# Kernel optimization log

Hardware: AMD Instinct MI355X
Metric: run time of the kernel (lower is better)

## Reference

```python
import jax, jax.numpy as jnp
import numpy as np

S, D, H = 1024, 512, 4
DK = D // H  # 128
POOL = 16
EPS = 1e-5


def _pos_encoding(seq_len, dmodel):
    pos = jnp.arange(seq_len, dtype=jnp.float32)[:, None]
    div = jnp.exp(jnp.arange(0, dmodel, 2, dtype=jnp.float32) * (-jnp.log(10000.0) / dmodel))
    ang = pos * div  # [S, D/2]
    # interleave sin/cos -> pe[:,0::2]=sin, pe[:,1::2]=cos
    return jnp.stack([jnp.sin(ang), jnp.cos(ang)], axis=-1).reshape(seq_len, dmodel)


def _layernorm(x, g, b):
    mu = jnp.mean(x, axis=-1, keepdims=True)
    var = jnp.var(x, axis=-1, keepdims=True)
    return (x - mu) * jax.lax.rsqrt(var + EPS) * g + b


def setup_inputs() -> dict:
    key = jax.random.key(0)
    ks = jax.random.split(key, 16)
    u = lambda k, shape, r: jax.random.uniform(k, shape, jnp.float32, -r, r)
    nfeature = 512
    return {
        "x": jax.random.normal(ks[0], (16, S, nfeature), jnp.float32),
        "emb_w": u(ks[1], (nfeature, D), (1.0 / nfeature) ** 0.5),
        "emb_b": u(ks[2], (D,), (1.0 / nfeature) ** 0.5),
        "WQ": u(ks[3], (H, D, DK), 0.1),
        "WK": u(ks[4], (H, D, DK), 0.1),
        "WV": u(ks[5], (H, D, DK), 0.1),
        "WO": u(ks[6], (H * DK, D), 0.1),
        "g1": jnp.ones((D,), jnp.float32),
        "b1": jnp.zeros((D,), jnp.float32),
        "l1_w": u(ks[7], (D, 4 * D), (1.0 / D) ** 0.5),
        "l1_b": u(ks[8], (4 * D,), (1.0 / D) ** 0.5),
        "l2_w": u(ks[9], (4 * D, D), (1.0 / (4 * D)) ** 0.5),
        "l2_b": u(ks[10], (D,), (1.0 / (4 * D)) ** 0.5),
        "g2": jnp.ones((D,), jnp.float32),
        "b2": jnp.zeros((D,), jnp.float32),
        "fc_w": u(ks[11], (S * (D // POOL), 2), 0.1),
        "fc_b": jnp.zeros((2,), jnp.float32),
    }


def reference(x, emb_w, emb_b, WQ, WK, WV, WO, g1, b1, l1_w, l1_b, l2_w, l2_b, g2, b2, fc_w, fc_b):
    # dropout layers are identity (eval mode)
    h = x @ emb_w + emb_b                       # [B,S,D]
    h = h.reshape(-1, S, D) + _pos_encoding(S, D)
    inp = h
    # per-head projections (hand-rolled MHA)
    Qi = jnp.einsum('bsd,hde->bhse', h, WQ)     # [B,H,S,DK]
    Ki = jnp.einsum('bsd,hde->bhse', h, WK)
    Vi = jnp.einsum('bsd,hde->bhse', h, WV)
    scores = jnp.einsum('bhse,bhte->bhst', Qi, Ki) / jnp.sqrt(jnp.float32(DK))
    attn = jax.nn.softmax(scores, axis=-1)      # [B,H,S,S] -- full attention matrix, as in source
    head = jnp.einsum('bhst,bhte->bhse', attn, Vi)  # [B,H,S,DK]
    # NOTE: source does a raw reshape [B,H,S,DK] -> [B,S,H*DK] (no transpose); replicate exactly
    out = head.reshape(-1, S, H * DK) @ WO      # [B,S,D]
    h = _layernorm(out + inp, g1, b1)
    ffn = jax.nn.relu(h @ l1_w + l1_b) @ l2_w + l2_b
    h = _layernorm(ffn + h, g2, b2)
    # MaxPool1d(16,16) over the feature dim: [B,S,512] -> [B,S,32]
    pooled = h.reshape(-1, S, D // POOL, POOL).max(axis=-1)
    logits = pooled.reshape(-1, S * (D // POOL)) @ fc_w + fc_b  # [B,2]
    return jax.nn.log_softmax(logits, axis=-1)
```

## Files before the change

kernel.cpp:

```cpp
#include <hip/hip_runtime.h>

typedef unsigned short ushortb;
typedef __attribute__((ext_vector_type(8))) short short8;
typedef __attribute__((ext_vector_type(4))) float f32x4;

__device__ __forceinline__ ushortb f2bb(float f) {
    union { float f; unsigned u; } x; x.f = f;
    unsigned r = x.u + 0x7fffu + ((x.u >> 16) & 1u);
    return (ushortb)(r >> 16);
}
__device__ __forceinline__ float bb2f(ushortb u) {
    union { unsigned u; float f; } x; x.u = ((unsigned)u) << 16; return x.f;
}

__device__ __forceinline__ void async_ld16(void* lds, const void* g) {
    __builtin_amdgcn_global_load_lds(
        (const __attribute__((address_space(1))) void*)g,
        (__attribute__((address_space(3))) void*)lds, 16, 0, 0);
}

#define EP_EMB       0
#define EP_RES       2
#define EP_BIAS_RELU 3
#define EP_BIAS_RES  4
#define EP_QKV       7

template <int EP>
__global__ __launch_bounds__(256) void gemm_mfma(
    const ushortb* __restrict__ A, const ushortb* __restrict__ Bt,
    const float* __restrict__ bias, const ushortb* __restrict__ res,
    const float* __restrict__ pe, ushortb* __restrict__ C,
    int M, int N, int K)
{
    __shared__ ushortb sA[128][64];
    __shared__ ushortb sB[128][64];

    const int tid = threadIdx.x;
    const int wave = tid >> 6, lane = tid & 63;
    const int quad = lane >> 4, l15 = lane & 15;
    const int row0 = blockIdx.x * 128;
    const int col0 = blockIdx.y * 128;
    const int wm = (wave >> 1) * 64, wn = (wave & 1) * 64;
    const int srl = lane >> 3, slot = lane & 7;

    f32x4 acc[4][4];
    #pragma unroll
    for (int i = 0; i < 4; ++i)
        #pragma unroll
        for (int j = 0; j < 4; ++j) acc[i][j] = (f32x4){0.f, 0.f, 0.f, 0.f};

    for (int k0 = 0; k0 < K; k0 += 64) {
        __syncthreads();
        #pragma unroll
        for (int c = 0; c < 4; ++c) {
            int rbase = wave * 32 + c * 8;
            int r = rbase + srl;
            int ka = (slot ^ ((r ^ (r >> 3)) & 7)) * 8;
            async_ld16(&sA[rbase][0], A  + (size_t)(row0 + r) * K + k0 + ka);
            async_ld16(&sB[rbase][0], Bt + (size_t)(col0 + r) * K + k0 + ka);
        }
        __syncthreads();

        #pragma unroll
        for (int kc = 0; kc < 2; ++kc) {
            short8 af[4], bf[4];
            #pragma unroll
            for (int i = 0; i < 4; ++i) {
                int m = wm + i * 16 + l15;
                af[i] = *(const short8*)&sA[m][(((kc * 4 + quad) ^ ((m ^ (m >> 3)) & 7))) * 8];
            }
            #pragma unroll
            for (int j = 0; j < 4; ++j) {
                int n = wn + j * 16 + l15;
                bf[j] = *(const short8*)&sB[n][(((kc * 4 + quad) ^ ((n ^ (n >> 3)) & 7))) * 8];
            }
            #pragma unroll
            for (int i = 0; i < 4; ++i)
                #pragma unroll
                for (int j = 0; j < 4; ++j)
                    acc[i][j] = __builtin_amdgcn_mfma_f32_16x16x32_bf16(af[i], bf[j], acc[i][j], 0, 0, 0);
        }
    }

    if constexpr (EP == EP_QKV) {
        if (col0 < 1024) {
            ushortb* dst = C + ((size_t)(col0 >> 9)) * ((size_t)M * 512);
            #pragma unroll
            for (int i = 0; i < 4; ++i) {
                #pragma unroll
                for (int r = 0; r < 4; ++r) {
                    int row = row0 + wm + i * 16 + quad * 4 + r;
                    #pragma unroll
                    for (int j = 0; j < 4; ++j) {
                        int col = (col0 + wn + j * 16 + l15) & 511;
                        dst[(size_t)row * 512 + col] = f2bb(acc[i][j][r]);
                    }
                }
            }
        } else {
            ushortb* Vt = C + (size_t)2 * M * 512;
            int bb = row0 >> 10;
            #pragma unroll
            for (int i = 0; i < 4; ++i) {
                int s = (row0 & 1023) + wm + i * 16 + quad * 4;
                #pragma unroll
                for (int j = 0; j < 4; ++j) {
                    int vcol = col0 + wn + j * 16 + l15 - 1024;
                    int h = vcol >> 7, e = vcol & 127;
                    ushort4 v;
                    v.x = f2bb(acc[i][j][0]); v.y = f2bb(acc[i][j][1]);
                    v.z = f2bb(acc[i][j][2]); v.w = f2bb(acc[i][j][3]);
                    *(ushort4*)&Vt[((size_t)((bb * 4 + h) * 128 + e) << 10) + s] = v;
                }
            }
        }
        return;
    }

    #pragma unroll
    for (int i = 0; i < 4; ++i) {
        #pragma unroll
        for (int r = 0; r < 4; ++r) {
            int row = row0 + wm + i * 16 + quad * 4 + r;
            #pragma unroll
            for (int j = 0; j < 4; ++j) {
                int col = col0 + wn + j * 16 + l15;
                float v = acc[i][j][r];
                if constexpr (EP == EP_EMB) {
                    v += bias[col] + pe[((row & 1023) << 9) + col];
                } else if constexpr (EP == EP_RES) {
                    v += bb2f(res[(size_t)row * N + col]);
                } else if constexpr (EP == EP_BIAS_RELU) {
                    v = fmaxf(v + bias[col], 0.0f);
                } else if constexpr (EP == EP_BIAS_RES) {
                    v += bias[col] + bb2f(res[(size_t)row * N + col]);
                }
                C[(size_t)row * N + col] = f2bb(v);
            }
        }
    }
}

__global__ __launch_bounds__(256) void conv_x(const float* __restrict__ in,
                                              ushortb* __restrict__ out)
{
    size_t i4 = (size_t)blockIdx.x * 256 + threadIdx.x;
    float4 v = *(const float4*)(in + i4 * 4);
    ushort4 o;
    o.x = f2bb(v.x); o.y = f2bb(v.y); o.z = f2bb(v.z); o.w = f2bb(v.w);
    *(ushort4*)(out + i4 * 4) = o;
}

__global__ __launch_bounds__(256) void tileT(const float* __restrict__ in,
                                             ushortb* __restrict__ out,
                                             int R, int C, float scale)
{
    __shared__ float t[64][65];
    const int tx = threadIdx.x & 63, ty = threadIdx.x >> 6;
    const int c0 = blockIdx.x * 64, r0 = blockIdx.y * 64;
    const size_t zoff = (size_t)blockIdx.z * R * C;
    #pragma unroll
    for (int i = 0; i < 16; ++i) {
        int r = ty + i * 4;
        t[r][tx] = in[zoff + (size_t)(r0 + r) * C + c0 + tx] * scale;
    }
    __syncthreads();
    #pragma unroll
    for (int i = 0; i < 16; ++i) {
        int r = ty + i * 4;
        out[zoff + (size_t)(c0 + r) * R + r0 + tx] = f2bb(t[tx][r]);
    }
}

__global__ __launch_bounds__(256) void pe_kernel(float* __restrict__ pe)
{
    int idx = blockIdx.x * 256 + threadIdx.x;
    int s = idx >> 9, c = idx & 511;
    float div = expf((float)(c & ~1) * (-9.210340371976184f / 512.0f));
    float ang = (float)s * div;
    pe[idx] = (c & 1) ? cosf(ang) : sinf(ang);
}

__global__ __launch_bounds__(256) void attn_mfma(
    const ushortb* __restrict__ Qb, const ushortb* __restrict__ Kb,
    const ushortb* __restrict__ Vt, ushortb* __restrict__ O)
{
    __shared__ ushortb sK[32][136];
    __shared__ ushortb sVt[128][40];
    __shared__ ushortb sP[4][32][40];

    const int tid = threadIdx.x;
    const int wave = tid >> 6, lane = tid & 63;
    const int quad = lane >> 4, l15 = lane & 15;
    const int b = blockIdx.z, h = blockIdx.y;
    const int q0 = blockIdx.x * 128 + wave * 32;
    const size_t qk_off = ((size_t)b << 10) * 512 + h * 128;
    const ushortb* Qp = Qb + qk_off;
    const ushortb* Kp = Kb + qk_off;
    const ushortb* Vp = Vt + (((size_t)(b * 4 + h)) << 17);

    short8 qfA[4], qfB[4];
    {
        const ushortb* qa = Qp + (size_t)(q0 + l15) * 512;
        const ushortb* qb = Qp + (size_t)(q0 + 16 + l15) * 512;
        #pragma unroll
        for (int kc = 0; kc < 4; ++kc) {
            qfA[kc] = *(const short8*)(qa + kc * 32 + quad * 8);
            qfB[kc] = *(const short8*)(qb + kc * 32 + quad * 8);
        }
    }

    f32x4 oA[8], oB[8];
    #pragma unroll
    for (int dt = 0; dt < 8; ++dt) {
        oA[dt] = (f32x4){0.f, 0.f, 0.f, 0.f};
        oB[dt] = (f32x4){0.f, 0.f, 0.f, 0.f};
    }
    float lA = 0.f, lB = 0.f;

    for (int t0 = 0; t0 < 1024; t0 += 32) {
        __syncthreads();
        #pragma unroll
        for (int c = 0; c < 2; ++c) {
            int idx = c * 2048 + tid * 8;
            int t = idx >> 7, d0 = idx & 127;
            *(short8*)&sK[t][d0] = *(const short8*)(Kp + (size_t)(t0 + t) * 512 + d0);
        }
        #pragma unroll
        for (int c = 0; c < 2; ++c) {
            int idx = c * 256 + tid;
            int d = idx >> 2, toff = (idx & 3) * 8;
            *(short8*)&sVt[d][toff] = *(const short8*)(Vp + ((size_t)d << 10) + t0 + toff);
        }
        __syncthreads();

        f32x4 sA0 = {0,0,0,0}, sA1 = {0,0,0,0}, sB0 = {0,0,0,0}, sB1 = {0,0,0,0};
        #pragma unroll
        for (int kc = 0; kc < 4; ++kc) {
            short8 k0f = *(const short8*)&sK[l15][kc * 32 + quad * 8];
            short8 k1f = *(const short8*)&sK[16 + l15][kc * 32 + quad * 8];
            sA0 = __builtin_amdgcn_mfma_f32_16x16x32_bf16(k0f, qfA[kc], sA0, 0, 0, 0);
            sA1 = __builtin_amdgcn_mfma_f32_16x16x32_bf16(k1f, qfA[kc], sA1, 0, 0, 0);
            sB0 = __builtin_amdgcn_mfma_f32_16x16x32_bf16(k0f, qfB[kc], sB0, 0, 0, 0);
            sB1 = __builtin_amdgcn_mfma_f32_16x16x32_bf16(k1f, qfB[kc], sB1, 0, 0, 0);
        }

        float pA0[4], pA1[4], pB0[4], pB1[4];
        float sumA = 0.f, sumB = 0.f;
        #pragma unroll
        for (int r = 0; r < 4; ++r) {
            pA0[r] = exp2f(sA0[r]); pA1[r] = exp2f(sA1[r]);
            pB0[r] = exp2f(sB0[r]); pB1[r] = exp2f(sB1[r]);
            sumA += pA0[r] + pA1[r];
            sumB += pB0[r] + pB1[r];
        }
        lA += sumA; lB += sumB;

        ushort4 w;
        w.x = f2bb(pA0[0]); w.y = f2bb(pA0[1]); w.z = f2bb(pA0[2]); w.w = f2bb(pA0[3]);
        *(ushort4*)&sP[wave][l15][quad * 4] = w;
        w.x = f2bb(pA1[0]); w.y = f2bb(pA1[1]); w.z = f2bb(pA1[2]); w.w = f2bb(pA1[3]);
        *(ushort4*)&sP[wave][l15][16 + quad * 4] = w;
        w.x = f2bb(pB0[0]); w.y = f2bb(pB0[1]); w.z = f2bb(pB0[2]); w.w = f2bb(pB0[3]);
        *(ushort4*)&sP[wave][16 + l15][quad * 4] = w;
        w.x = f2bb(pB1[0]); w.y = f2bb(pB1[1]); w.z = f2bb(pB1[2]); w.w = f2bb(pB1[3]);
        *(ushort4*)&sP[wave][16 + l15][16 + quad * 4] = w;

        short8 pfA = *(const short8*)&sP[wave][l15][quad * 8];
        short8 pfB = *(const short8*)&sP[wave][16 + l15][quad * 8];

        #pragma unroll
        for (int dt = 0; dt < 8; ++dt) {
            short8 vfrag = *(const short8*)&sVt[dt * 16 + l15][quad * 8];
            oA[dt] = __builtin_amdgcn_mfma_f32_16x16x32_bf16(pfA, vfrag, oA[dt], 0, 0, 0);
            oB[dt] = __builtin_amdgcn_mfma_f32_16x16x32_bf16(pfB, vfrag, oB[dt], 0, 0, 0);
        }
    }

    lA += __shfl_xor(lA, 16); lA += __shfl_xor(lA, 32);
    lB += __shfl_xor(lB, 16); lB += __shfl_xor(lB, 32);

    const size_t obase = (((size_t)(b * 4 + h) << 10) + q0) << 7;
    #pragma unroll
    for (int r = 0; r < 4; ++r) {
        float invA = 1.0f / __shfl(lA, quad * 4 + r);
        float invB = 1.0f / __shfl(lB, quad * 4 + r);
        int qa = quad * 4 + r, qb = 16 + quad * 4 + r;
        #pragma unroll
        for (int dt = 0; dt < 8; ++dt) {
            O[obase + ((size_t)qa << 7) + dt * 16 + l15] = f2bb(oA[dt][r] * invA);
            O[obase + ((size_t)qb << 7) + dt * 16 + l15] = f2bb(oB[dt][r] * invB);
        }
    }
}

__global__ __launch_bounds__(256) void ln_kernel(const ushortb* __restrict__ in,
                                                 const float* __restrict__ g,
                                                 const float* __restrict__ bta,
                                                 ushortb* __restrict__ out)
{
    const int lane = threadIdx.x & 63, w = threadIdx.x >> 6;
    const size_t row = (size_t)blockIdx.x * 4 + w;
    const int e0 = lane * 8;
    short8 v8 = *(const short8*)(in + row * 512 + e0);
    float v[8];
    #pragma unroll
    for (int k = 0; k < 8; ++k) v[k] = bb2f((ushortb)((short*)&v8)[k]);
    float s = 0.f, sq = 0.f;
    #pragma unroll
    for (int k = 0; k < 8; ++k) { s += v[k]; sq += v[k] * v[k]; }
    #pragma unroll
    for (int o = 1; o < 64; o <<= 1) { s += __shfl_xor(s, o); sq += __shfl_xor(sq, o); }
    float mu = s * (1.0f / 512.0f);
    float var = sq * (1.0f / 512.0f) - mu * mu;
    float rstd = rsqrtf(var + 1e-5f);
    float4 g0 = *(const float4*)(g + e0),  g1 = *(const float4*)(g + e0 + 4);
    float4 b0 = *(const float4*)(bta + e0), b1 = *(const float4*)(bta + e0 + 4);
    float gg[8] = {g0.x, g0.y, g0.z, g0.w, g1.x, g1.y, g1.z, g1.w};
    float bb[8] = {b0.x, b0.y, b0.z, b0.w, b1.x, b1.y, b1.z, b1.w};
    short8 o8;
    #pragma unroll
    for (int k = 0; k < 8; ++k)
        ((short*)&o8)[k] = (short)f2bb((v[k] - mu) * rstd * gg[k] + bb[k]);
    *(short8*)(out + row * 512 + e0) = o8;
}

__global__ __launch_bounds__(256) void final_partial(const ushortb* __restrict__ ln2,
                                                     const float* __restrict__ fcw,
                                                     float* __restrict__ zbuf)
{
    const int b = blockIdx.x, chunk = blockIdx.y;
    const int tid = threadIdx.x;
    float a0 = 0.0f, a1 = 0.0f;
    #pragma unroll
    for (int t = 0; t < 8; ++t) {
        int m = chunk * 2048 + t * 256 + tid;
        int s = m >> 5, j = m & 31;
        const ushortb* p = ln2 + (((size_t)(b * 1024 + s)) << 9) + j * 16;
        float mx = -1e30f;
        #pragma unroll
        for (int e = 0; e < 16; ++e) mx = fmaxf(mx, bb2f(p[e]));
        a0 += mx * fcw[2 * m];
        a1 += mx * fcw[2 * m + 1];
    }
    __shared__ float r0[256], r1[256];
    r0[tid] = a0; r1[tid] = a1;
    __syncthreads();
    for (int o = 128; o > 0; o >>= 1) {
        if (tid < o) { r0[tid] += r0[tid + o]; r1[tid] += r1[tid + o]; }
        __syncthreads();
    }
    if (tid == 0) {
        atomicAdd(&zbuf[2 * b],     r0[0]);
        atomicAdd(&zbuf[2 * b + 1], r1[0]);
    }
}

__global__ __launch_bounds__(64) void final_logits(const float* __restrict__ zbuf,
                                                   const float* __restrict__ fcb,
                                                   float* __restrict__ out)
{
    int b = threadIdx.x;
    if (b < 16) {
        float z0 = zbuf[2 * b]     + fcb[0];
        float z1 = zbuf[2 * b + 1] + fcb[1];
        float mx = fmaxf(z0, z1);
        float lse = mx + logf(expf(z0 - mx) + expf(z1 - mx));
        out[2 * b]     = z0 - lse;
        out[2 * b + 1] = z1 - lse;
    }
}

extern "C" void kernel_launch(void* const* d_in, const int* in_sizes, int n_in,
                              void* d_out, int out_size, void* d_ws, size_t ws_size,
                              hipStream_t stream)
{
    const float* x     = (const float*)d_in[0];
    const float* emb_w = (const float*)d_in[1];
    const float* emb_b = (const float*)d_in[2];
    const float* WQ    = (const float*)d_in[3];
    const float* WK    = (const float*)d_in[4];
    const float* WV    = (const float*)d_in[5];
    const float* WO    = (const float*)d_in[6];
    const float* g1    = (const float*)d_in[7];
    const float* b1    = (const float*)d_in[8];
    const float* l1w   = (const float*)d_in[9];
    const float* l1b   = (const float*)d_in[10];
    const float* l2w   = (const float*)d_in[11];
    const float* l2b   = (const float*)d_in[12];
    const float* g2    = (const float*)d_in[13];
    const float* b2    = (const float*)d_in[14];
    const float* fcw   = (const float*)d_in[15];
    const float* fcb   = (const float*)d_in[16];
    float* out = (float*)d_out;

    char* ws = (char*)d_ws;
    const size_t Ub = (size_t)16384 * 512 * 2;
    ushortb* xb    = (ushortb*)(ws + 0 * Ub);
    ushortb* h0b   = (ushortb*)(ws + 1 * Ub);
    ushortb* Qb    = (ushortb*)(ws + 2 * Ub);
    ushortb* Kb    = (ushortb*)(ws + 3 * Ub);
    ushortb* Vt    = (ushortb*)(ws + 4 * Ub);
    ushortb* headR = (ushortb*)(ws + 5 * Ub);
    ushortb* mid   = (ushortb*)(ws + 3 * Ub);
    ushortb* r1    = xb;
    ushortb* ln1   = Qb;
    ushortb* r2    = xb;
    ushortb* ln2   = h0b;
    char* wb = ws + 7 * Ub;
    ushortb* embwt = (ushortb*)(wb);
    ushortb* wqkvt = (ushortb*)(wb + 524288);
    ushortb* wot   = (ushortb*)(wb + 2097152);
    ushortb* l1wt  = (ushortb*)(wb + 2621440);
    ushortb* l2wt  = (ushortb*)(wb + 4718592);
    float*   pe    = (float*)  (wb + 6815744);
    float*   zbuf  = (float*)  (wb + 8912896);

    const int M = 16384;
    const float qscale = 0.12753139626997592f;

    conv_x<<<8192, 256, 0, stream>>>(x, xb);
    pe_kernel<<<2048, 256, 0, stream>>>(pe);
    tileT<<<dim3(8, 8, 1),  256, 0, stream>>>(emb_w, embwt, 512, 512, 1.0f);
    tileT<<<dim3(2, 8, 4),  256, 0, stream>>>(WQ, wqkvt,               512, 128, qscale);
    tileT<<<dim3(2, 8, 4),  256, 0, stream>>>(WK, wqkvt + 262144,      512, 128, 1.0f);
    tileT<<<dim3(2, 8, 4),  256, 0, stream>>>(WV, wqkvt + 524288,      512, 128, 1.0f);
    tileT<<<dim3(8, 8, 1),  256, 0, stream>>>(WO, wot, 512, 512, 1.0f);
    tileT<<<dim3(32, 8, 1), 256, 0, stream>>>(l1w, l1wt, 512, 2048, 1.0f);
    tileT<<<dim3(8, 32, 1), 256, 0, stream>>>(l2w, l2wt, 2048, 512, 1.0f);
    hipMemsetAsync(zbuf, 0, 16 * 2 * sizeof(float), stream);

    gemm_mfma<EP_EMB><<<dim3(M / 128, 4), 256, 0, stream>>>(
        xb, embwt, emb_b, nullptr, pe, h0b, M, 512, 512);

    gemm_mfma<EP_QKV><<<dim3(M / 128, 12), 256, 0, stream>>>(
        h0b, wqkvt, nullptr, nullptr, nullptr, Qb, M, 1536, 512);

    attn_mfma<<<dim3(8, 4, 16), 256, 0, stream>>>(Qb, Kb, Vt, headR);

    gemm_mfma<EP_RES><<<dim3(M / 128, 4), 256, 0, stream>>>(
        headR, wot, nullptr, h0b, nullptr, r1, M, 512, 512);
    ln_kernel<<<M / 4, 256, 0, stream>>>(r1, g1, b1, ln1);

    gemm_mfma<EP_BIAS_RELU><<<dim3(M / 128, 16), 256, 0, stream>>>(
        ln1, l1wt, l1b, nullptr, nullptr, mid, M, 2048, 512);
    gemm_mfma<EP_BIAS_RES><<<dim3(M / 128, 4), 256, 0, stream>>>(
        mid, l2wt, l2b, ln1, nullptr, r2, M, 512, 2048);
    ln_kernel<<<M / 4, 256, 0, stream>>>(r2, g2, b2, ln2);

    final_partial<<<dim3(16, 16), 256, 0, stream>>>(ln2, fcw, zbuf);
    final_logits<<<1, 64, 0, stream>>>(zbuf, fcb, out);
}
```

Before: 390.4 us.

## Fold embedding into QKV weights and fuse embedding with QKV GEMM

Precomputes the product of the QKV projection weights and the embedding weights, plus a positional-encoding/bias table projected through QKV. A single GEMM over x then produces h0 and Q/K/V directly, removing the dependent embedding-to-QKV GEMM chain and one full activation round trip. The attention kernel now loads K/V tiles with async global-to-LDS copies into XOR-swizzled unpadded shared arrays, and uses a flat block index that puts heads of the same batch in adjacent blocks. The precomposed weights and tables are rounded to bf16, which changes numerics slightly.

Measured after the change: 408.6 us. 4.7% more time.

```diff
diff --git a/kernel.cpp b/kernel.cpp
--- a/kernel.cpp
+++ b/kernel.cpp
@@ -19,18 +19,18 @@
         (__attribute__((address_space(3))) void*)lds, 16, 0, 0);
 }
 
-#define EP_EMB       0
+#define EP_ST        1
 #define EP_RES       2
 #define EP_BIAS_RELU 3
 #define EP_BIAS_RES  4
-#define EP_QKV       7
+#define EP_MEGA      8
 
 template <int EP>
 __global__ __launch_bounds__(256) void gemm_mfma(
     const ushortb* __restrict__ A, const ushortb* __restrict__ Bt,
     const float* __restrict__ bias, const ushortb* __restrict__ res,
-    const float* __restrict__ pe, ushortb* __restrict__ C,
-    int M, int N, int K)
+    const ushortb* __restrict__ tab1, const ushortb* __restrict__ tab2,
+    ushortb* __restrict__ C, int M, int N, int K)
 {
     __shared__ ushortb sA[128][64];
     __shared__ ushortb sB[128][64];
@@ -82,35 +82,53 @@
         }
     }
 
-    if constexpr (EP == EP_QKV) {
-        if (col0 < 1024) {
-            ushortb* dst = C + ((size_t)(col0 >> 9)) * ((size_t)M * 512);
-            #pragma unroll
-            for (int i = 0; i < 4; ++i) {
+    if constexpr (EP == EP_MEGA) {
+        if (col0 < 512) {
+            #pragma unroll
+            for (int i = 0; i < 4; ++i)
                 #pragma unroll
                 for (int r = 0; r < 4; ++r) {
                     int row = row0 + wm + i * 16 + quad * 4 + r;
+                    int s = row & 1023;
                     #pragma unroll
                     for (int j = 0; j < 4; ++j) {
-                        int col = (col0 + wn + j * 16 + l15) & 511;
-                        dst[(size_t)row * 512 + col] = f2bb(acc[i][j][r]);
+                        int col = col0 + wn + j * 16 + l15;
+                        C[(size_t)row * 512 + col] =
+                            f2bb(acc[i][j][r] + bb2f(tab1[(s << 9) + col]));
                     }
                 }
-            }
+        } else if (col0 < 1536) {
+            int sec = (col0 - 512) >> 9;
+            ushortb* dst = C + (size_t)(1 + sec) * M * 512;
+            #pragma unroll
+            for (int i = 0; i < 4; ++i)
+                #pragma unroll
+                for (int r = 0; r < 4; ++r) {
+                    int row = row0 + wm + i * 16 + quad * 4 + r;
+                    int s = row & 1023;
+                    #pragma unroll
+                    for (int j = 0; j < 4; ++j) {
+                        int cn = col0 + wn + j * 16 + l15 - 512;
+                        dst[(size_t)row * 512 + (cn & 511)] =
+                            f2bb(acc[i][j][r] + bb2f(tab2[(size_t)s * 1536 + cn]));
+                    }
+                }
         } else {
-            ushortb* Vt = C + (size_t)2 * M * 512;
-            int bb = row0 >> 10;
+            ushortb* Vt = C + (size_t)3 * M * 512;
+            int bb_ = row0 >> 10;
             #pragma unroll
             for (int i = 0; i < 4; ++i) {
-                int s = (row0 & 1023) + wm + i * 16 + quad * 4;
+                int sb = (row0 & 1023) + wm + i * 16 + quad * 4;
                 #pragma unroll
                 for (int j = 0; j < 4; ++j) {
-                    int vcol = col0 + wn + j * 16 + l15 - 1024;
-                    int h = vcol >> 7, e = vcol & 127;
+                    int cn = col0 + wn + j * 16 + l15 - 512;
+                    int e = cn & 127, hh = (cn - 1024) >> 7;
                     ushort4 v;
-                    v.x = f2bb(acc[i][j][0]); v.y = f2bb(acc[i][j][1]);
-                    v.z = f2bb(acc[i][j][2]); v.w = f2bb(acc[i][j][3]);
-                    *(ushort4*)&Vt[((size_t)((bb * 4 + h) * 128 + e) << 10) + s] = v;
+                    v.x = f2bb(acc[i][j][0] + bb2f(tab2[(size_t)(sb + 0) * 1536 + cn]));
+                    v.y = f2bb(acc[i][j][1] + bb2f(tab2[(size_t)(sb + 1) * 1536 + cn]));
+                    v.z = f2bb(acc[i][j][2] + bb2f(tab2[(size_t)(sb + 2) * 1536 + cn]));
+                    v.w = f2bb(acc[i][j][3] + bb2f(tab2[(size_t)(sb + 3) * 1536 + cn]));
+                    *(ushort4*)&Vt[((size_t)((bb_ * 4 + hh) * 128 + e) << 10) + sb] = v;
                 }
             }
         }
@@ -126,9 +144,7 @@
             for (int j = 0; j < 4; ++j) {
                 int col = col0 + wn + j * 16 + l15;
                 float v = acc[i][j][r];
-                if constexpr (EP == EP_EMB) {
-                    v += bias[col] + pe[((row & 1023) << 9) + col];
-                } else if constexpr (EP == EP_RES) {
+                if constexpr (EP == EP_RES) {
                     v += bb2f(res[(size_t)row * N + col]);
                 } else if constexpr (EP == EP_BIAS_RELU) {
                     v = fmaxf(v + bias[col], 0.0f);
@@ -141,7 +157,7 @@
     }
 }
 
-__global__ __launch_bounds__(256) void conv_x(const float* __restrict__ in,
+__global__ __launch_bounds__(256) void conv_b(const float* __restrict__ in,
                                               ushortb* __restrict__ out)
 {
     size_t i4 = (size_t)blockIdx.x * 256 + threadIdx.x;
@@ -172,28 +188,32 @@
     }
 }
 
-__global__ __launch_bounds__(256) void pe_kernel(float* __restrict__ pe)
+__global__ __launch_bounds__(256) void peb_kernel(const float* __restrict__ emb_b,
+                                                  ushortb* __restrict__ peb)
 {
     int idx = blockIdx.x * 256 + threadIdx.x;
     int s = idx >> 9, c = idx & 511;
     float div = expf((float)(c & ~1) * (-9.210340371976184f / 512.0f));
     float ang = (float)s * div;
-    pe[idx] = (c & 1) ? cosf(ang) : sinf(ang);
+    float v = ((c & 1) ? cosf(ang) : sinf(ang)) + emb_b[c];
+    peb[idx] = f2bb(v);
 }
 
 __global__ __launch_bounds__(256) void attn_mfma(
     const ushortb* __restrict__ Qb, const ushortb* __restrict__ Kb,
     const ushortb* __restrict__ Vt, ushortb* __restrict__ O)
 {
-    __shared__ ushortb sK[32][136];
-    __shared__ ushortb sVt[128][40];
+    __shared__ ushortb sK[32][128];
+    __shared__ ushortb sVt[128][32];
     __shared__ ushortb sP[4][32][40];
 
     const int tid = threadIdx.x;
     const int wave = tid >> 6, lane = tid & 63;
     const int quad = lane >> 4, l15 = lane & 15;
-    const int b = blockIdx.z, h = blockIdx.y;
-    const int q0 = blockIdx.x * 128 + wave * 32;
+    const int bid = blockIdx.x;
+    const int bh = bid & 63, qc = bid >> 6;
+    const int b = bh >> 2, h = bh & 3;
+    const int q0 = qc * 128 + wave * 32;
     const size_t qk_off = ((size_t)b << 10) * 512 + h * 128;
     const ushortb* Qp = Qb + qk_off;
     const ushortb* Kp = Kb + qk_off;
@@ -222,23 +242,21 @@
         __syncthreads();
         #pragma unroll
         for (int c = 0; c < 2; ++c) {
-            int idx = c * 2048 + tid * 8;
-            int t = idx >> 7, d0 = idx & 127;
-            *(short8*)&sK[t][d0] = *(const short8*)(Kp + (size_t)(t0 + t) * 512 + d0);
-        }
-        #pragma unroll
-        for (int c = 0; c < 2; ++c) {
-            int idx = c * 256 + tid;
-            int d = idx >> 2, toff = (idx & 3) * 8;
-            *(short8*)&sVt[d][toff] = *(const short8*)(Vp + ((size_t)d << 10) + t0 + toff);
+            int seg = wave * 2 + c;
+            int rk = seg * 4 + (lane >> 4);
+            int ck = (lane & 15) ^ (rk & 15);
+            async_ld16(&sK[seg * 4][0], Kp + (size_t)(t0 + rk) * 512 + ck * 8);
+            int dv = seg * 16 + (lane >> 2);
+            int cv = (lane & 3) ^ (dv & 3);
+            async_ld16(&sVt[seg * 16][0], Vp + ((size_t)dv << 10) + t0 + cv * 8);
         }
         __syncthreads();
 
         f32x4 sA0 = {0,0,0,0}, sA1 = {0,0,0,0}, sB0 = {0,0,0,0}, sB1 = {0,0,0,0};
         #pragma unroll
         for (int kc = 0; kc < 4; ++kc) {
-            short8 k0f = *(const short8*)&sK[l15][kc * 32 + quad * 8];
-            short8 k1f = *(const short8*)&sK[16 + l15][kc * 32 + quad * 8];
+            short8 k0f = *(const short8*)&sK[l15][((kc * 4 + quad) ^ l15) * 8];
+            short8 k1f = *(const short8*)&sK[16 + l15][((kc * 4 + quad) ^ l15) * 8];
             sA0 = __builtin_amdgcn_mfma_f32_16x16x32_bf16(k0f, qfA[kc], sA0, 0, 0, 0);
             sA1 = __builtin_amdgcn_mfma_f32_16x16x32_bf16(k1f, qfA[kc], sA1, 0, 0, 0);
             sB0 = __builtin_amdgcn_mfma_f32_16x16x32_bf16(k0f, qfB[kc], sB0, 0, 0, 0);
@@ -271,7 +289,8 @@
 
         #pragma unroll
         for (int dt = 0; dt < 8; ++dt) {
-            short8 vfrag = *(const short8*)&sVt[dt * 16 + l15][quad * 8];
+            int d = dt * 16 + l15;
+            short8 vfrag = *(const short8*)&sVt[d][(quad ^ (d & 3)) * 8];
             oA[dt] = __builtin_amdgcn_mfma_f32_16x16x32_bf16(pfA, vfrag, oA[dt], 0, 0, 0);
             oB[dt] = __builtin_amdgcn_mfma_f32_16x16x32_bf16(pfB, vfrag, oB[dt], 0, 0, 0);
         }
@@ -408,44 +427,50 @@
     ushortb* r2    = xb;
     ushortb* ln2   = h0b;
     char* wb = ws + 7 * Ub;
-    ushortb* embwt = (ushortb*)(wb);
-    ushortb* wqkvt = (ushortb*)(wb + 524288);
-    ushortb* wot   = (ushortb*)(wb + 2097152);
-    ushortb* l1wt  = (ushortb*)(wb + 2621440);
-    ushortb* l2wt  = (ushortb*)(wb + 4718592);
-    float*   pe    = (float*)  (wb + 6815744);
-    float*   zbuf  = (float*)  (wb + 8912896);
+    ushortb* WB    = (ushortb*)(wb);
+    ushortb* W2t   = WB + (size_t)512 * 512;
+    ushortb* wqkvt = (ushortb*)(wb + 2097152);
+    ushortb* embc  = (ushortb*)(wb + 3670016);
+    ushortb* wot   = (ushortb*)(wb + 4194304);
+    ushortb* l1wt  = (ushortb*)(wb + 4718592);
+    ushortb* l2wt  = (ushortb*)(wb + 6815744);
+    ushortb* peb   = (ushortb*)(wb + 8912896);
+    ushortb* peqkv = (ushortb*)(wb + 9961472);
+    float*   zbuf  = (float*)  (wb + 13107200);
 
     const int M = 16384;
     const float qscale = 0.12753139626997592f;
 
-    conv_x<<<8192, 256, 0, stream>>>(x, xb);
-    pe_kernel<<<2048, 256, 0, stream>>>(pe);
-    tileT<<<dim3(8, 8, 1),  256, 0, stream>>>(emb_w, embwt, 512, 512, 1.0f);
-    tileT<<<dim3(2, 8, 4),  256, 0, stream>>>(WQ, wqkvt,               512, 128, qscale);
-    tileT<<<dim3(2, 8, 4),  256, 0, stream>>>(WK, wqkvt + 262144,      512, 128, 1.0f);
-    tileT<<<dim3(2, 8, 4),  256, 0, stream>>>(WV, wqkvt + 524288,      512, 128, 1.0f);
+    conv_b<<<8192, 256, 0, stream>>>(x, xb);
+    conv_b<<<256, 256, 0, stream>>>(emb_w, embc);
+    peb_kernel<<<2048, 256, 0, stream>>>(emb_b, peb);
+    tileT<<<dim3(8, 8, 1),  256, 0, stream>>>(emb_w, WB, 512, 512, 1.0f);
+    tileT<<<dim3(2, 8, 4),  256, 0, stream>>>(WQ, wqkvt,          512, 128, qscale);
+    tileT<<<dim3(2, 8, 4),  256, 0, stream>>>(WK, wqkvt + 262144, 512, 128, 1.0f);
+    tileT<<<dim3(2, 8, 4),  256, 0, stream>>>(WV, wqkvt + 524288, 512, 128, 1.0f);
     tileT<<<dim3(8, 8, 1),  256, 0, stream>>>(WO, wot, 512, 512, 1.0f);
     tileT<<<dim3(32, 8, 1), 256, 0, stream>>>(l1w, l1wt, 512, 2048, 1.0f);
     tileT<<<dim3(8, 32, 1), 256, 0, stream>>>(l2w, l2wt, 2048, 512, 1.0f);
     hipMemsetAsync(zbuf, 0, 16 * 2 * sizeof(float), stream);
 
-    gemm_mfma<EP_EMB><<<dim3(M / 128, 4), 256, 0, stream>>>(
-        xb, embwt, emb_b, nullptr, pe, h0b, M, 512, 512);
-
-    gemm_mfma<EP_QKV><<<dim3(M / 128, 12), 256, 0, stream>>>(
-        h0b, wqkvt, nullptr, nullptr, nullptr, Qb, M, 1536, 512);
-
-    attn_mfma<<<dim3(8, 4, 16), 256, 0, stream>>>(Qb, Kb, Vt, headR);
+    gemm_mfma<EP_ST><<<dim3(12, 4), 256, 0, stream>>>(
+        wqkvt, embc, nullptr, nullptr, nullptr, nullptr, W2t, 1536, 512, 512);
+    gemm_mfma<EP_ST><<<dim3(8, 12), 256, 0, stream>>>(
+        peb, wqkvt, nullptr, nullptr, nullptr, nullptr, peqkv, 1024, 1536, 512);
+
+    gemm_mfma<EP_MEGA><<<dim3(M / 128, 16), 256, 0, stream>>>(
+        xb, WB, nullptr, nullptr, peb, peqkv, h0b, M, 2048, 512);
+
+    attn_mfma<<<512, 256, 0, stream>>>(Qb, Kb, Vt, headR);
 
     gemm_mfma<EP_RES><<<dim3(M / 128, 4), 256, 0, stream>>>(
-        headR, wot, nullptr, h0b, nullptr, r1, M, 512, 512);
+        headR, wot, nullptr, h0b, nullptr, nullptr, r1, M, 512, 512);
     ln_kernel<<<M / 4, 256, 0, stream>>>(r1, g1, b1, ln1);
 
     gemm_mfma<EP_BIAS_RELU><<<dim3(M / 128, 16), 256, 0, stream>>>(
-        ln1, l1wt, l1b, nullptr, nullptr, mid, M, 2048, 512);
+        ln1, l1wt, l1b, nullptr, nullptr, nullptr, mid, M, 2048, 512);
     gemm_mfma<EP_BIAS_RES><<<dim3(M / 128, 4), 256, 0, stream>>>(
-        mid, l2wt, l2b, ln1, nullptr, r2, M, 512, 2048);
+        mid, l2wt, l2b, ln1, nullptr, nullptr, r2, M, 512, 2048);
     ln_kernel<<<M / 4, 256, 0, stream>>>(r2, g2, b2, ln2);
 
     final_partial<<<dim3(16, 16), 256, 0, stream>>>(ln2, fcw, zbuf);
```

## Double-buffer LDS tiles in GEMM and attention to overlap loads with MFMA

Applied to the files above, without the earlier changes.

The GEMM main loop now uses two LDS buffers. The next K-tile is prefetched with global_load_lds while MFMAs run on the current one, which leaves one barrier per iteration instead of two. The attention kernel gets the same treatment: K and V^T tiles move to double-buffered async LDS loads, and an XOR swizzle replaces the row padding to avoid bank conflicts. The attention grid is also flattened to 1D so that blocks sharing a batch and head are spread differently across CUs. In exchange, GEMM LDS use doubles to 64KB per block, which can lower occupancy.

New measurement: 367.3 us. 5.9% less time.

```diff
diff --git a/kernel.cpp b/kernel.cpp
--- a/kernel.cpp
+++ b/kernel.cpp
@@ -32,8 +32,8 @@
     const float* __restrict__ pe, ushortb* __restrict__ C,
     int M, int N, int K)
 {
-    __shared__ ushortb sA[128][64];
-    __shared__ ushortb sB[128][64];
+    __shared__ ushortb sA[2][128][64];
+    __shared__ ushortb sB[2][128][64];
 
     const int tid = threadIdx.x;
     const int wave = tid >> 6, lane = tid & 63;
@@ -49,30 +49,41 @@
         #pragma unroll
         for (int j = 0; j < 4; ++j) acc[i][j] = (f32x4){0.f, 0.f, 0.f, 0.f};
 
+    #pragma unroll
+    for (int c = 0; c < 4; ++c) {
+        int rbase = wave * 32 + c * 8;
+        int r = rbase + srl;
+        int ka = (slot ^ ((r ^ (r >> 3)) & 7)) * 8;
+        async_ld16(&sA[0][rbase][0], A  + (size_t)(row0 + r) * K + ka);
+        async_ld16(&sB[0][rbase][0], Bt + (size_t)(col0 + r) * K + ka);
+    }
+
+    int buf = 0;
     for (int k0 = 0; k0 < K; k0 += 64) {
         __syncthreads();
-        #pragma unroll
-        for (int c = 0; c < 4; ++c) {
-            int rbase = wave * 32 + c * 8;
-            int r = rbase + srl;
-            int ka = (slot ^ ((r ^ (r >> 3)) & 7)) * 8;
-            async_ld16(&sA[rbase][0], A  + (size_t)(row0 + r) * K + k0 + ka);
-            async_ld16(&sB[rbase][0], Bt + (size_t)(col0 + r) * K + k0 + ka);
-        }
-        __syncthreads();
-
+        if (k0 + 64 < K) {
+            int nb = buf ^ 1;
+            #pragma unroll
+            for (int c = 0; c < 4; ++c) {
+                int rbase = wave * 32 + c * 8;
+                int r = rbase + srl;
+                int ka = (slot ^ ((r ^ (r >> 3)) & 7)) * 8;
+                async_ld16(&sA[nb][rbase][0], A  + (size_t)(row0 + r) * K + k0 + 64 + ka);
+                async_ld16(&sB[nb][rbase][0], Bt + (size_t)(col0 + r) * K + k0 + 64 + ka);
+            }
+        }
         #pragma unroll
         for (int kc = 0; kc < 2; ++kc) {
             short8 af[4], bf[4];
             #pragma unroll
             for (int i = 0; i < 4; ++i) {
                 int m = wm + i * 16 + l15;
-                af[i] = *(const short8*)&sA[m][(((kc * 4 + quad) ^ ((m ^ (m >> 3)) & 7))) * 8];
+                af[i] = *(const short8*)&sA[buf][m][(((kc * 4 + quad) ^ ((m ^ (m >> 3)) & 7))) * 8];
             }
             #pragma unroll
             for (int j = 0; j < 4; ++j) {
                 int n = wn + j * 16 + l15;
-                bf[j] = *(const short8*)&sB[n][(((kc * 4 + quad) ^ ((n ^ (n >> 3)) & 7))) * 8];
+                bf[j] = *(const short8*)&sB[buf][n][(((kc * 4 + quad) ^ ((n ^ (n >> 3)) & 7))) * 8];
             }
             #pragma unroll
             for (int i = 0; i < 4; ++i)
@@ -80,13 +91,14 @@
                 for (int j = 0; j < 4; ++j)
                     acc[i][j] = __builtin_amdgcn_mfma_f32_16x16x32_bf16(af[i], bf[j], acc[i][j], 0, 0, 0);
         }
+        buf ^= 1;
     }
 
     if constexpr (EP == EP_QKV) {
         if (col0 < 1024) {
             ushortb* dst = C + ((size_t)(col0 >> 9)) * ((size_t)M * 512);
             #pragma unroll
-            for (int i = 0; i < 4; ++i) {
+            for (int i = 0; i < 4; ++i)
                 #pragma unroll
                 for (int r = 0; r < 4; ++r) {
                     int row = row0 + wm + i * 16 + quad * 4 + r;
@@ -96,10 +108,9 @@
                         dst[(size_t)row * 512 + col] = f2bb(acc[i][j][r]);
                     }
                 }
-            }
         } else {
             ushortb* Vt = C + (size_t)2 * M * 512;
-            int bb = row0 >> 10;
+            int bb_ = row0 >> 10;
             #pragma unroll
             for (int i = 0; i < 4; ++i) {
                 int s = (row0 & 1023) + wm + i * 16 + quad * 4;
@@ -110,7 +121,7 @@
                     ushort4 v;
                     v.x = f2bb(acc[i][j][0]); v.y = f2bb(acc[i][j][1]);
                     v.z = f2bb(acc[i][j][2]); v.w = f2bb(acc[i][j][3]);
-                    *(ushort4*)&Vt[((size_t)((bb * 4 + h) * 128 + e) << 10) + s] = v;
+                    *(ushort4*)&Vt[((size_t)((bb_ * 4 + h) * 128 + e) << 10) + s] = v;
                 }
             }
         }
@@ -185,15 +196,17 @@
     const ushortb* __restrict__ Qb, const ushortb* __restrict__ Kb,
     const ushortb* __restrict__ Vt, ushortb* __restrict__ O)
 {
-    __shared__ ushortb sK[32][136];
-    __shared__ ushortb sVt[128][40];
+    __shared__ ushortb sK[2][32][128];
+    __shared__ ushortb sVt[2][128][32];
     __shared__ ushortb sP[4][32][40];
 
     const int tid = threadIdx.x;
     const int wave = tid >> 6, lane = tid & 63;
     const int quad = lane >> 4, l15 = lane & 15;
-    const int b = blockIdx.z, h = blockIdx.y;
-    const int q0 = blockIdx.x * 128 + wave * 32;
+    const int bid = blockIdx.x;
+    const int bh = bid & 63, qc = bid >> 6;
+    const int b = bh >> 2, h = bh & 3;
+    const int q0 = qc * 128 + wave * 32;
     const size_t qk_off = ((size_t)b << 10) * 512 + h * 128;
     const ushortb* Qp = Qb + qk_off;
     const ushortb* Kp = Kb + qk_off;
@@ -218,27 +231,39 @@
     }
     float lA = 0.f, lB = 0.f;
 
+    #pragma unroll
+    for (int c = 0; c < 2; ++c) {
+        int seg = wave * 2 + c;
+        int rk = seg * 4 + (lane >> 4);
+        int ck = (lane & 15) ^ (rk & 15);
+        async_ld16(&sK[0][seg * 4][0], Kp + (size_t)rk * 512 + ck * 8);
+        int dv = seg * 16 + (lane >> 2);
+        int cv = (lane & 3) ^ (dv & 3);
+        async_ld16(&sVt[0][seg * 16][0], Vp + ((size_t)dv << 10) + cv * 8);
+    }
+
+    int buf = 0;
     for (int t0 = 0; t0 < 1024; t0 += 32) {
         __syncthreads();
-        #pragma unroll
-        for (int c = 0; c < 2; ++c) {
-            int idx = c * 2048 + tid * 8;
-            int t = idx >> 7, d0 = idx & 127;
-            *(short8*)&sK[t][d0] = *(const short8*)(Kp + (size_t)(t0 + t) * 512 + d0);
-        }
-        #pragma unroll
-        for (int c = 0; c < 2; ++c) {
-            int idx = c * 256 + tid;
-            int d = idx >> 2, toff = (idx & 3) * 8;
-            *(short8*)&sVt[d][toff] = *(const short8*)(Vp + ((size_t)d << 10) + t0 + toff);
-        }
-        __syncthreads();
+        if (t0 + 32 < 1024) {
+            int nb = buf ^ 1;
+            #pragma unroll
+            for (int c = 0; c < 2; ++c) {
+                int seg = wave * 2 + c;
+                int rk = seg * 4 + (lane >> 4);
+                int ck = (lane & 15) ^ (rk & 15);
+                async_ld16(&sK[nb][seg * 4][0], Kp + (size_t)(t0 + 32 + rk) * 512 + ck * 8);
+                int dv = seg * 16 + (lane >> 2);
+                int cv = (lane & 3) ^ (dv & 3);
+                async_ld16(&sVt[nb][seg * 16][0], Vp + ((size_t)dv << 10) + t0 + 32 + cv * 8);
+            }
+        }
 
         f32x4 sA0 = {0,0,0,0}, sA1 = {0,0,0,0}, sB0 = {0,0,0,0}, sB1 = {0,0,0,0};
         #pragma unroll
         for (int kc = 0; kc < 4; ++kc) {
-            short8 k0f = *(const short8*)&sK[l15][kc * 32 + quad * 8];
-            short8 k1f = *(const short8*)&sK[16 + l15][kc * 32 + quad * 8];
+            short8 k0f = *(const short8*)&sK[buf][l15][((kc * 4 + quad) ^ l15) * 8];
+            short8 k1f = *(const short8*)&sK[buf][16 + l15][((kc * 4 + quad) ^ l15) * 8];
             sA0 = __builtin_amdgcn_mfma_f32_16x16x32_bf16(k0f, qfA[kc], sA0, 0, 0, 0);
             sA1 = __builtin_amdgcn_mfma_f32_16x16x32_bf16(k1f, qfA[kc], sA1, 0, 0, 0);
             sB0 = __builtin_amdgcn_mfma_f32_16x16x32_bf16(k0f, qfB[kc], sB0, 0, 0, 0);
@@ -271,10 +296,12 @@
 
         #pragma unroll
         for (int dt = 0; dt < 8; ++dt) {
-            short8 vfrag = *(const short8*)&sVt[dt * 16 + l15][quad * 8];
+            int d = dt * 16 + l15;
+            short8 vfrag = *(const short8*)&sVt[buf][d][(quad ^ (d & 3)) * 8];
             oA[dt] = __builtin_amdgcn_mfma_f32_16x16x32_bf16(pfA, vfrag, oA[dt], 0, 0, 0);
             oB[dt] = __builtin_amdgcn_mfma_f32_16x16x32_bf16(pfB, vfrag, oB[dt], 0, 0, 0);
         }
+        buf ^= 1;
     }
 
     lA += __shfl_xor(lA, 16); lA += __shfl_xor(lA, 32);
@@ -422,9 +449,9 @@
     conv_x<<<8192, 256, 0, stream>>>(x, xb);
     pe_kernel<<<2048, 256, 0, stream>>>(pe);
     tileT<<<dim3(8, 8, 1),  256, 0, stream>>>(emb_w, embwt, 512, 512, 1.0f);
-    tileT<<<dim3(2, 8, 4),  256, 0, stream>>>(WQ, wqkvt,               512, 128, qscale);
-    tileT<<<dim3(2, 8, 4),  256, 0, stream>>>(WK, wqkvt + 262144,      512, 128, 1.0f);
-    tileT<<<dim3(2, 8, 4),  256, 0, stream>>>(WV, wqkvt + 524288,      512, 128, 1.0f);
+    tileT<<<dim3(2, 8, 4),  256, 0, stream>>>(WQ, wqkvt,          512, 128, qscale);
+    tileT<<<dim3(2, 8, 4),  256, 0, stream>>>(WK, wqkvt + 262144, 512, 128, 1.0f);
+    tileT<<<dim3(2, 8, 4),  256, 0, stream>>>(WV, wqkvt + 524288, 512, 128, 1.0f);
     tileT<<<dim3(8, 8, 1),  256, 0, stream>>>(WO, wot, 512, 512, 1.0f);
     tileT<<<dim3(32, 8, 1), 256, 0, stream>>>(l1w, l1wt, 512, 2048, 1.0f);
     tileT<<<dim3(8, 32, 1), 256, 0, stream>>>(l2w, l2wt, 2048, 512, 1.0f);
@@ -436,7 +463,7 @@
     gemm_mfma<EP_QKV><<<dim3(M / 128, 12), 256, 0, stream>>>(
         h0b, wqkvt, nullptr, nullptr, nullptr, Qb, M, 1536, 512);
 
-    attn_mfma<<<dim3(8, 4, 16), 256, 0, stream>>>(Qb, Kb, Vt, headR);
+    attn_mfma<<<512, 256, 0, stream>>>(Qb, Kb, Vt, headR);
 
     gemm_mfma<EP_RES><<<dim3(M / 128, 4), 256, 0, stream>>>(
         headR, wot, nullptr, h0b, nullptr, r1, M, 512, 512);
```
